# Kernel optimization log

Measured on AMD Instinct MI355X. Metric: run time of the kernel, lower is better.

Reference implementation:

```python
import jax, jax.numpy as jnp
import numpy as np

NUM_NODES = 50000
NUM_EDGES = 800000
NUM_FEATURES = 128
HIDDEN = 256
NUM_CLASSES = 10
NUM_GRAPHS = 64


def setup_inputs() -> dict:
    key = jax.random.key(0)
    ks = jax.random.split(key, 16)
    x = jax.random.normal(ks[0], (NUM_NODES, NUM_FEATURES), dtype=jnp.float32)
    edge_index = jax.random.randint(ks[1], (2, NUM_EDGES), 0, NUM_NODES, dtype=jnp.int64)
    batch = jnp.sort(jax.random.randint(ks[2], (NUM_NODES,), 0, NUM_GRAPHS, dtype=jnp.int64))

    def glorot(k, shape):
        fan_in, fan_out = shape[-2], shape[-1]
        s = jnp.sqrt(6.0 / (fan_in + fan_out)).astype(jnp.float32)
        return jax.random.uniform(k, shape, jnp.float32, -s, s)

    inp = {
        "x": x, "edge_index": edge_index, "batch": batch,
        # Chebyshev weights: one [in, out] matrix per hop order k
        "W1": glorot(ks[3], (3, NUM_FEATURES, HIDDEN)), "b1": jnp.zeros((HIDDEN,), jnp.float32),
        "W2": glorot(ks[4], (4, HIDDEN, HIDDEN)),       "b2": jnp.zeros((HIDDEN,), jnp.float32),
        "W3": glorot(ks[5], (5, HIDDEN, HIDDEN)),       "b3": jnp.zeros((HIDDEN,), jnp.float32),
        "fc1_w": glorot(ks[6], (HIDDEN, 512)),  "fc1_b": jnp.zeros((512,), jnp.float32),
        "fc2_w": glorot(ks[7], (512, HIDDEN)),  "fc2_b": jnp.zeros((HIDDEN,), jnp.float32),
        "fc3_w": glorot(ks[8], (HIDDEN, NUM_CLASSES)), "fc3_b": jnp.zeros((NUM_CLASSES,), jnp.float32),
    }
    return inp


def reference(x, edge_index, batch, W1, b1, W2, b2, W3, b3,
              fc1_w, fc1_b, fc2_w, fc2_b, fc3_w, fc3_b):
    N = x.shape[0]
    src, dst = edge_index[0], edge_index[1]

    # Scaled Laplacian L_hat = -D^{-1/2} A D^{-1/2} (lambda_max = 2, sym norm)
    deg = jax.ops.segment_sum(jnp.ones_like(src, dtype=x.dtype), src, num_segments=N)
    dis = jnp.where(deg > 0, jax.lax.rsqrt(jnp.maximum(deg, 1.0)), 0.0)
    w = -dis[src] * dis[dst]  # [E]

    def prop(h):  # L_hat @ h via gather-scale-scatter
        return jax.ops.segment_sum(h[src] * w[:, None], dst, num_segments=N)

    def cheb(h, Wk, b):
        K = Wk.shape[0]
        Tx0 = h
        out = Tx0 @ Wk[0]
        Tx1 = prop(h)
        out = out + Tx1 @ Wk[1]
        for k in range(2, K):
            Tx2 = 2.0 * prop(Tx1) - Tx0
            out = out + Tx2 @ Wk[k]
            Tx0, Tx1 = Tx1, Tx2
        return out + b

    h = jax.nn.relu(cheb(x, W1, b1))
    h = jax.nn.relu(cheb(h, W2, b2))
    h = jax.nn.relu(cheb(h, W3, b3))

    # global mean pool over graphs in the batch
    sums = jax.ops.segment_sum(h, batch, num_segments=NUM_GRAPHS)
    cnts = jax.ops.segment_sum(jnp.ones((N,), h.dtype), batch, num_segments=NUM_GRAPHS)
    g = sums / jnp.maximum(cnts, 1.0)[:, None]  # [G, 256]

    g = jax.nn.relu(g @ fc1_w + fc1_b)  # dropout is identity at inference
    g = jax.nn.relu(g @ fc2_w + fc2_b)
    g = g @ fc3_w + fc3_b
    return jax.nn.log_softmax(g, axis=1)
```

## Files before the change

kernel.cpp:

```cpp
#include <hip/hip_runtime.h>
#include <cstdint>
#include <cstddef>

#define NN 50000
#define NE 800000
#define FIN 128
#define HID 256
#define NCLS 10
#define NG 64
#define LDT 1280

#define NCH 13
#define NCELL (NN * NCH)
#define NSCB ((NCELL + 255) / 256)

typedef unsigned int uint;
typedef unsigned short ushort;
typedef __attribute__((ext_vector_type(8))) short short8;
typedef __attribute__((ext_vector_type(4))) float f32x4;

static inline size_t align_up(size_t v, size_t a) { return (v + a - 1) / a * a; }

__device__ __forceinline__ float bf2f(ushort u) {
    union { uint i; float f; } v; v.i = (uint)u << 16; return v.f;
}
__device__ __forceinline__ ushort f2bf(float f) {
    union { uint i; float f; } v; v.f = f;
    uint i = v.i;
    uint r = (i + 0x7fffu + ((i >> 16) & 1u)) >> 16;
    return (ushort)r;
}
__device__ __forceinline__ uint pack2(float a, float b) {
    return (uint)f2bf(a) | ((uint)f2bf(b) << 16);
}


__global__ void k_degcnt(const int* __restrict__ src, const int* __restrict__ dst,
                         int* __restrict__ ideg, uint* __restrict__ cellcnt32) {
    int e = blockIdx.x * 256 + threadIdx.x;
    if (e < NE) {
        int s = src[e], d = dst[e];
        atomicAdd(&ideg[s], 1);
        int cell = d * NCH + (s >> 12);
        atomicAdd(&cellcnt32[cell >> 1], 1u << ((cell & 1) * 16));
    }
}

__global__ void k_dis(const int* __restrict__ ideg, float* __restrict__ dis) {
    int n = blockIdx.x * 256 + threadIdx.x;
    if (n < NN) {
        int d = ideg[n];
        dis[n] = (d > 0) ? rsqrtf((float)d) : 0.0f;
    }
}

__global__ void k_scanA(const uint* __restrict__ cnt32, int* __restrict__ rp,
                        int* __restrict__ bsum) {
    __shared__ int s[256];
    int i = blockIdx.x * 256 + threadIdx.x;
    int v = 0;
    if (i < NCELL) v = (int)((cnt32[i >> 1] >> ((i & 1) * 16)) & 0xffffu);
    s[threadIdx.x] = v;
    __syncthreads();
    for (int off = 1; off < 256; off <<= 1) {
        int t = (threadIdx.x >= (unsigned)off) ? s[threadIdx.x - off] : 0;
        __syncthreads();
        s[threadIdx.x] += t;
        __syncthreads();
    }
    if (i < NCELL) rp[i] = s[threadIdx.x] - v;
    if (threadIdx.x == 255) bsum[blockIdx.x] = s[255];
}

__global__ void k_scanB(int* __restrict__ b, int n) {
    __shared__ int s[1024];
    __shared__ int carry;
    if (threadIdx.x == 0) carry = 0;
    __syncthreads();
    for (int base = 0; base < n; base += 1024) {
        int i = base + threadIdx.x;
        int v = (i < n) ? b[i] : 0;
        s[threadIdx.x] = v;
        __syncthreads();
        for (int off = 1; off < 1024; off <<= 1) {
            int t = (threadIdx.x >= (unsigned)off) ? s[threadIdx.x - off] : 0;
            __syncthreads();
            s[threadIdx.x] += t;
            __syncthreads();
        }
        int c = carry;
        if (i < n) b[i] = c + s[threadIdx.x] - v;
        __syncthreads();
        if (threadIdx.x == 0) carry = c + s[1023];
        __syncthreads();
    }
}

__global__ void k_scanC(const int* __restrict__ bsum, int* __restrict__ rp,
                        int* __restrict__ rpn) {
    int i = blockIdx.x * 256 + threadIdx.x;
    if (i < NCELL) {
        int v = rp[i] + bsum[blockIdx.x];
        rp[i] = v;
        if (i % NCH == 0) rpn[i / NCH] = v;
    }
    if (i == 0) rpn[NN] = NE;
}

__global__ void k_fill2(const int* __restrict__ src, const int* __restrict__ dst,
                        const float* __restrict__ dis,
                        const int* __restrict__ cellptr, uint* __restrict__ cur32,
                        uint2* __restrict__ em) {
    int e = blockIdx.x * 256 + threadIdx.x;
    if (e < NE) {
        int s = src[e], d = dst[e];
        int cell = d * NCH + (s >> 12);
        uint old = atomicAdd(&cur32[cell >> 1], 1u << ((cell & 1) * 16));
        int loc = (int)((old >> ((cell & 1) * 16)) & 0xffffu);
        uint2 m;
        m.x = (uint)s;
        m.y = __float_as_uint(-dis[s] * dis[d]);
        em[cellptr[cell] + loc] = m;
    }
}

__global__ void k_wtall(const float* __restrict__ W1, const float* __restrict__ W2,
                        const float* __restrict__ W3, ushort* __restrict__ Wt1,
                        ushort* __restrict__ Wt2, ushort* __restrict__ Wt3) {
    int i = blockIdx.x * 256 + threadIdx.x;
    if (i < 384 * 256) {
        int k = i >> 8, n = i & 255;
        Wt1[(size_t)n * 384 + k] = f2bf(W1[i]);
        return;
    }
    i -= 384 * 256;
    if (i < 1024 * 256) {
        int k = i >> 8, n = i & 255;
        Wt2[(size_t)n * 1024 + k] = f2bf(W2[i]);
        return;
    }
    i -= 1024 * 256;
    if (i < 1280 * 256) {
        int k = i >> 8, n = i & 255;
        Wt3[(size_t)n * 1280 + k] = f2bf(W3[i]);
    }
}


__global__ void k_spread_x(const float* __restrict__ x, ushort* __restrict__ T) {
    int i = blockIdx.x * 256 + threadIdx.x;
    if (i < NN * 64) {
        int m = i >> 6, p = i & 63;
        const float* xp = x + (size_t)m * FIN + p * 2;
        uint* tp = (uint*)(T + (size_t)m * LDT) + p;
        *tp = pack2(xp[0], xp[1]);
    }
}

template <int FUSE, int F>
__global__ __launch_bounds__(512) void k_prop3(
    const int* __restrict__ rpn, const uint2* __restrict__ em,
    const ushort* __restrict__ h, const ushort* __restrict__ sub,
    ushort* __restrict__ out) {
    constexpr int NV = (F == 256) ? 4 : 2;
    int wv = __builtin_amdgcn_readfirstlane(threadIdx.x >> 6);
    int d = blockIdx.x * 8 + wv;
    int lane = threadIdx.x & 63;
    int beg = rpn[d], end = rpn[d + 1];
    float a[NV];
#pragma unroll
    for (int j = 0; j < NV; ++j) a[j] = 0.0f;

    int e = beg;
    int nfull = (end - beg) >> 3;
    if (nfull > 0) {
        uint2 mt[8];
#pragma unroll
        for (int u = 0; u < 8; ++u) mt[u] = em[e + u];
        for (int g = 0; g < nfull; ++g) {
            uint2 mtn[8];
            if (F == 256) {
                uint2 gg[8];
#pragma unroll
                for (int u = 0; u < 8; ++u)
                    gg[u] = *((const uint2*)(h + (size_t)mt[u].x * LDT) + lane);
#pragma unroll
                for (int u = 0; u < 8; ++u) {
                    int pe = e + 8 + u; if (pe > end - 1) pe = end - 1;
                    mtn[u] = em[pe];
                }
#pragma unroll
                for (int u = 0; u < 8; ++u) {
                    float wvv = __uint_as_float(mt[u].y);
                    a[0] += wvv * bf2f((ushort)gg[u].x);
                    a[1] += wvv * bf2f((ushort)(gg[u].x >> 16));
                    a[2] += wvv * bf2f((ushort)gg[u].y);
                    a[3] += wvv * bf2f((ushort)(gg[u].y >> 16));
                }
            } else {
                uint gg[8];
#pragma unroll
                for (int u = 0; u < 8; ++u)
                    gg[u] = *((const uint*)(h + (size_t)mt[u].x * LDT) + lane);
#pragma unroll
                for (int u = 0; u < 8; ++u) {
                    int pe = e + 8 + u; if (pe > end - 1) pe = end - 1;
                    mtn[u] = em[pe];
                }
#pragma unroll
                for (int u = 0; u < 8; ++u) {
                    float wvv = __uint_as_float(mt[u].y);
                    a[0] += wvv * bf2f((ushort)gg[u]);
                    a[1] += wvv * bf2f((ushort)(gg[u] >> 16));
                }
            }
#pragma unroll
            for (int u = 0; u < 8; ++u) mt[u] = mtn[u];
            e += 8;
        }
    }
    for (; e + 4 <= end; e += 4) {
        uint2 mt[4];
#pragma unroll
        for (int u = 0; u < 4; ++u) mt[u] = em[e + u];
        if (F == 256) {
            uint2 gg[4];
#pragma unroll
            for (int u = 0; u < 4; ++u)
                gg[u] = *((const uint2*)(h + (size_t)mt[u].x * LDT) + lane);
#pragma unroll
            for (int u = 0; u < 4; ++u) {
                float wvv = __uint_as_float(mt[u].y);
                a[0] += wvv * bf2f((ushort)gg[u].x);
                a[1] += wvv * bf2f((ushort)(gg[u].x >> 16));
                a[2] += wvv * bf2f((ushort)gg[u].y);
                a[3] += wvv * bf2f((ushort)(gg[u].y >> 16));
            }
        } else {
            uint gg[4];
#pragma unroll
            for (int u = 0; u < 4; ++u)
                gg[u] = *((const uint*)(h + (size_t)mt[u].x * LDT) + lane);
#pragma unroll
            for (int u = 0; u < 4; ++u) {
                float wvv = __uint_as_float(mt[u].y);
                a[0] += wvv * bf2f((ushort)gg[u]);
                a[1] += wvv * bf2f((ushort)(gg[u] >> 16));
            }
        }
    }
    for (; e < end; ++e) {
        uint2 m0 = em[e];
        float w0 = __uint_as_float(m0.y);
        if (F == 256) {
            uint2 g0 = *((const uint2*)(h + (size_t)m0.x * LDT) + lane);
            a[0] += w0 * bf2f((ushort)g0.x); a[1] += w0 * bf2f((ushort)(g0.x >> 16));
            a[2] += w0 * bf2f((ushort)g0.y); a[3] += w0 * bf2f((ushort)(g0.y >> 16));
        } else {
            uint g0 = *((const uint*)(h + (size_t)m0.x * LDT) + lane);
            a[0] += w0 * bf2f((ushort)g0); a[1] += w0 * bf2f((ushort)(g0 >> 16));
        }
    }

    if (F == 256) {
        uint2* op = (uint2*)(out + (size_t)d * LDT) + lane;
        if (FUSE) {
            uint2 sv = *((const uint2*)(sub + (size_t)d * LDT) + lane);
            uint2 r;
            r.x = pack2(2.0f * a[0] - bf2f((ushort)sv.x),
                        2.0f * a[1] - bf2f((ushort)(sv.x >> 16)));
            r.y = pack2(2.0f * a[2] - bf2f((ushort)sv.y),
                        2.0f * a[3] - bf2f((ushort)(sv.y >> 16)));
            *op = r;
        } else {
            uint2 r;
            r.x = pack2(a[0], a[1]);
            r.y = pack2(a[2], a[3]);
            *op = r;
        }
    } else {
        uint* op = (uint*)(out + (size_t)d * LDT) + lane;
        if (FUSE) {
            uint sv = *((const uint*)(sub + (size_t)d * LDT) + lane);
            *op = pack2(2.0f * a[0] - bf2f((ushort)sv),
                        2.0f * a[1] - bf2f((ushort)(sv >> 16)));
        } else {
            *op = pack2(a[0], a[1]);
        }
    }
}

template <int K>
__global__ __launch_bounds__(512, 4) void k_mm7(
    const ushort* __restrict__ A, int lda,
    int m0, int m1, int m2, int m3, int m4,
    const ushort* __restrict__ Wt, const float* __restrict__ bias,
    ushort* __restrict__ H, int ldh, int M) {
    constexpr int NT = K / 32;
    __shared__ ushort As[3][128 * 32];
    __shared__ ushort Bs[3][256 * 32];
    int tid = threadIdx.x;
    int lane = tid & 63, w = tid >> 6;
    int wm = w >> 2, wn = w & 3;
    int rowBase = blockIdx.x * 128;
    int srow = lane >> 2;
    int c16 = lane & 3;

    f32x4 acc[4][4];
#pragma unroll
    for (int i = 0; i < 4; ++i)
#pragma unroll
        for (int j = 0; j < 4; ++j) acc[i][j] = (f32x4){0.f, 0.f, 0.f, 0.f};

    auto stage = [&](int t) {
        int kk = t * 32;
        int slot = kk >> 8;
        int coff = (slot == 0 ? m0 : slot == 1 ? m1 : slot == 2 ? m2
                    : slot == 3 ? m3 : m4) + (kk & 255);
        int b = t % 3;
        {
            int r = w * 16 + srow;
            int cs = c16 ^ ((r >> 1) & 3);
            int grow = rowBase + r;
            if (grow > M - 1) grow = M - 1;
            const ushort* gp = A + (size_t)grow * lda + coff + cs * 8;
            __builtin_amdgcn_global_load_lds(
                (const __attribute__((address_space(1))) void*)gp,
                (__attribute__((address_space(3))) void*)((char*)&As[b][0] + w * 1024),
                16, 0, 0);
        }
#pragma unroll
        for (int q = 0; q < 2; ++q) {
            int seg = w * 2 + q;
            int r = seg * 16 + srow;
            int cs = c16 ^ ((r >> 1) & 3);
            const ushort* gp = Wt + (size_t)r * K + kk + cs * 8;
            __builtin_amdgcn_global_load_lds(
                (const __attribute__((address_space(1))) void*)gp,
                (__attribute__((address_space(3))) void*)((char*)&Bs[b][0] + seg * 1024),
                16, 0, 0);
        }
    };

    stage(0);
    stage(1);

    for (int t = 0; t < NT; ++t) {
        if (t + 1 < NT) {
            asm volatile("s_waitcnt vmcnt(3)" ::: "memory");
        } else {
            asm volatile("s_waitcnt vmcnt(0)" ::: "memory");
        }
        __builtin_amdgcn_s_barrier();
        if (t + 2 < NT) stage(t + 2);

        int b = t % 3;
        short8 af[4], bf[4];
#pragma unroll
        for (int mi = 0; mi < 4; ++mi) {
            int r = wm * 64 + mi * 16 + (lane & 15);
            int j = (lane >> 4) ^ ((r >> 1) & 3);
            af[mi] = *(const short8*)((const char*)&As[b][0] + r * 64 + j * 16);
        }
#pragma unroll
        for (int ni = 0; ni < 4; ++ni) {
            int r = wn * 64 + ni * 16 + (lane & 15);
            int j = (lane >> 4) ^ ((r >> 1) & 3);
            bf[ni] = *(const short8*)((const char*)&Bs[b][0] + r * 64 + j * 16);
        }
#pragma unroll
        for (int mi = 0; mi < 4; ++mi)
#pragma unroll
            for (int ni = 0; ni < 4; ++ni)
                acc[mi][ni] = __builtin_amdgcn_mfma_f32_16x16x32_bf16(
                    af[mi], bf[ni], acc[mi][ni], 0, 0, 0);
    }

    int lg = lane >> 4;
    float bv[4];
#pragma unroll
    for (int ni = 0; ni < 4; ++ni)
        bv[ni] = bias[wn * 64 + ni * 16 + (lane & 15)];
#pragma unroll
    for (int mi = 0; mi < 4; ++mi) {
#pragma unroll
        for (int r = 0; r < 4; ++r) {
            int row = rowBase + wm * 64 + mi * 16 + lg * 4 + r;
            if (row >= M) continue;
#pragma unroll
            for (int ni = 0; ni < 4; ++ni) {
                int colL = wn * 64 + ni * 16 + (lane & 15);
                float v = acc[mi][ni][r] + bv[ni];
                v = fmaxf(v, 0.0f);
                H[(size_t)row * ldh + colL] = f2bf(v);
            }
        }
    }
}


__global__ void k_pool(const ushort* __restrict__ h, const int* __restrict__ batch,
                       float* __restrict__ sums, float* __restrict__ cnts) {
    int f = threadIdx.x;
    int n0 = blockIdx.x * 128;
    if (n0 >= NN) return;
    int nEnd = n0 + 128 < NN ? n0 + 128 : NN;
    int cur = batch[n0];
    float acc = 0.0f, c = 0.0f;
    for (int n = n0; n < nEnd; ++n) {
        int b = batch[n];
        if (b != cur) {
            atomicAdd(&sums[cur * HID + f], acc);
            if (f == 0) atomicAdd(&cnts[cur], c);
            acc = 0.0f; c = 0.0f; cur = b;
        }
        acc += bf2f(h[(size_t)n * HID + f]);
        c += 1.0f;
    }
    atomicAdd(&sums[cur * HID + f], acc);
    if (f == 0) atomicAdd(&cnts[cur], c);
}

__global__ void k_gdiv(const float* __restrict__ sums, const float* __restrict__ cnts,
                       float* __restrict__ g) {
    int i = blockIdx.x * 256 + threadIdx.x;
    int b = i >> 8;
    g[i] = sums[i] / fmaxf(cnts[b], 1.0f);
}


template <int RELU>
__global__ void k_fc(const float* __restrict__ in, const float* __restrict__ W,
                     const float* __restrict__ bias, float* __restrict__ out,
                     int K, int Nc) {
    __shared__ float s[512];
    int gi = blockIdx.x;
    for (int i = threadIdx.x; i < K; i += blockDim.x) s[i] = in[gi * K + i];
    __syncthreads();
    int c = blockIdx.y * blockDim.x + threadIdx.x;
    if (c < Nc) {
        float acc = bias[c];
        for (int k = 0; k < K; ++k) acc += s[k] * W[k * Nc + c];
        out[gi * Nc + c] = RELU ? fmaxf(acc, 0.0f) : acc;
    }
}

__global__ void k_fc3_lsm(const float* __restrict__ in, const float* __restrict__ W,
                          const float* __restrict__ b, float* __restrict__ out) {
    __shared__ float s[HID];
    __shared__ float lg[NCLS];
    int gi = blockIdx.x;
    s[threadIdx.x] = in[gi * HID + threadIdx.x];
    __syncthreads();
    if (threadIdx.x < NCLS) {
        float acc = b[threadIdx.x];
        for (int k = 0; k < HID; ++k) acc += s[k] * W[k * NCLS + threadIdx.x];
        lg[threadIdx.x] = acc;
    }
    __syncthreads();
    if (threadIdx.x < NCLS) {
        float m = -1e30f;
        for (int c = 0; c < NCLS; ++c) m = fmaxf(m, lg[c]);
        float sum = 0.0f;
        for (int c = 0; c < NCLS; ++c) sum += expf(lg[c] - m);
        out[gi * NCLS + threadIdx.x] = lg[threadIdx.x] - m - logf(sum);
    }
}


extern "C" void kernel_launch(void* const* d_in, const int* in_sizes, int n_in,
                              void* d_out, int out_size, void* d_ws, size_t ws_size,
                              hipStream_t stream) {
    const float* x = (const float*)d_in[0];
    const int* ei = (const int*)d_in[1];
    const int* src = ei;
    const int* dst = ei + NE;
    const int* batch = (const int*)d_in[2];
    const float* W1 = (const float*)d_in[3];
    const float* b1 = (const float*)d_in[4];
    const float* W2 = (const float*)d_in[5];
    const float* b2 = (const float*)d_in[6];
    const float* W3 = (const float*)d_in[7];
    const float* b3 = (const float*)d_in[8];
    const float* fc1w = (const float*)d_in[9];
    const float* fc1b = (const float*)d_in[10];
    const float* fc2w = (const float*)d_in[11];
    const float* fc2b = (const float*)d_in[12];
    const float* fc3w = (const float*)d_in[13];
    const float* fc3b = (const float*)d_in[14];
    float* out = (float*)d_out;

    char* p = (char*)d_ws;
    auto carve = [&](size_t bytes) {
        char* r = p;
        p += align_up(bytes, 256);
        return (void*)r;
    };
    ushort* Tbig = (ushort*)carve((size_t)NN * LDT * 2);
    ushort* hA = (ushort*)carve((size_t)NN * HID * 2);
    ushort* Wt1 = (ushort*)carve((size_t)HID * 384 * 2);
    ushort* Wt2 = (ushort*)carve((size_t)HID * 1024 * 2);
    ushort* Wt3 = (ushort*)carve((size_t)HID * 1280 * 2);
    int* ideg = (int*)carve((size_t)NN * 4);
    float* dis = (float*)carve((size_t)NN * 4);
    uint2* em = (uint2*)carve((size_t)NE * 8);
    uint* cellcnt32 = (uint*)carve((size_t)NCELL * 2);
    int* cellptr = (int*)carve((size_t)(NCELL + 1) * 4);
    uint* cur32 = (uint*)carve((size_t)NCELL * 2);
    int* rpn = (int*)carve((size_t)(NN + 1) * 4);
    int* bsum = (int*)carve((size_t)NSCB * 4);
    float* psum = (float*)carve((size_t)NG * HID * 4);
    float* pcnt = (float*)carve((size_t)NG * 4);
    float* g = (float*)carve((size_t)NG * HID * 4);
    float* f1 = (float*)carve((size_t)NG * 512 * 4);
    float* f2 = (float*)carve((size_t)NG * HID * 4);

    hipMemsetAsync(ideg, 0, (size_t)NN * 4, stream);
    hipMemsetAsync(cellcnt32, 0, (size_t)NCELL * 2, stream);
    hipMemsetAsync(cur32, 0, (size_t)NCELL * 2, stream);
    hipMemsetAsync(psum, 0, (size_t)NG * HID * 4, stream);
    hipMemsetAsync(pcnt, 0, (size_t)NG * 4, stream);

    k_degcnt<<<(NE + 255) / 256, 256, 0, stream>>>(src, dst, ideg, cellcnt32);
    k_dis<<<(NN + 255) / 256, 256, 0, stream>>>(ideg, dis);
    k_scanA<<<NSCB, 256, 0, stream>>>(cellcnt32, cellptr, bsum);
    k_scanB<<<1, 1024, 0, stream>>>(bsum, NSCB);
    k_scanC<<<NSCB, 256, 0, stream>>>(bsum, cellptr, rpn);
    k_fill2<<<(NE + 255) / 256, 256, 0, stream>>>(src, dst, dis, cellptr, cur32, em);

    k_wtall<<<(384 + 1024 + 1280), 256, 0, stream>>>(W1, W2, W3, Wt1, Wt2, Wt3);

    int mmg = (NN + 127) / 128;

    k_spread_x<<<(NN * 64 + 255) / 256, 256, 0, stream>>>(x, Tbig);
    k_prop3<0, 128><<<NN / 8, 512, 0, stream>>>(rpn, em, Tbig + 0, nullptr, Tbig + 128);
    k_prop3<1, 128><<<NN / 8, 512, 0, stream>>>(rpn, em, Tbig + 128, Tbig + 0, Tbig + 256);
    k_mm7<384><<<mmg, 512, 0, stream>>>(Tbig, LDT, 0, 256, 0, 0, 0,
                                        Wt1, b1, Tbig + 1024, LDT, NN);

    k_prop3<0, 256><<<NN / 8, 512, 0, stream>>>(rpn, em, Tbig + 1024, nullptr, Tbig + 0);
    k_prop3<1, 256><<<NN / 8, 512, 0, stream>>>(rpn, em, Tbig + 0, Tbig + 1024, Tbig + 256);
    k_prop3<1, 256><<<NN / 8, 512, 0, stream>>>(rpn, em, Tbig + 256, Tbig + 0, Tbig + 512);
    k_mm7<1024><<<mmg, 512, 0, stream>>>(Tbig, LDT, 1024, 0, 256, 512, 0,
                                         Wt2, b2, Tbig + 768, LDT, NN);

    k_prop3<0, 256><<<NN / 8, 512, 0, stream>>>(rpn, em, Tbig + 768, nullptr, Tbig + 1024);
    k_prop3<1, 256><<<NN / 8, 512, 0, stream>>>(rpn, em, Tbig + 1024, Tbig + 768, Tbig + 0);
    k_prop3<1, 256><<<NN / 8, 512, 0, stream>>>(rpn, em, Tbig + 0, Tbig + 1024, Tbig + 256);
    k_prop3<1, 256><<<NN / 8, 512, 0, stream>>>(rpn, em, Tbig + 256, Tbig + 0, Tbig + 512);
    k_mm7<1280><<<mmg, 512, 0, stream>>>(Tbig, LDT, 768, 1024, 0, 256, 512,
                                         Wt3, b3, hA, HID, NN);

    k_pool<<<(NN + 127) / 128, 256, 0, stream>>>(hA, batch, psum, pcnt);
    k_gdiv<<<(NG * HID) / 256, 256, 0, stream>>>(psum, pcnt, g);
    k_fc<1><<<dim3(NG, 2), 256, 0, stream>>>(g, fc1w, fc1b, f1, HID, 512);
    k_fc<1><<<dim3(NG, 1), 256, 0, stream>>>(f1, fc2w, fc2b, f2, 512, HID);
    k_fc3_lsm<<<NG, 256, 0, stream>>>(f2, fc3w, fc3b, out);
}
```

Baseline: 797.0 us.

## Widen 256-feature gathers to 16B half-wave loads and fuse preprocessing kernels

The 256-feature propagation kernel now splits each wavefront into two half-waves. Each half loads a full 512-byte row with 16-byte loads for alternating edges, and the partial sums are combined with a cross-half shuffle. This gives fewer, wider gather loads per edge and avoids the 4-edge tail loop. Preprocessing is also consolidated: degree counting records each edge's rank within its cell, which removes the second atomic pass and the cur32 buffer. The dis computation is merged into the scan kernel, and the edge fill, weight transpose and x conversion are merged into one launch. In exchange the kernel adds register pressure, a shuffle reduction and an odd-edge tail handled by masking.

```diff
diff --git a/kernel.cpp b/kernel.cpp
--- a/kernel.cpp
+++ b/kernel.cpp
@@ -13,6 +13,11 @@
 #define NCH 13
 #define NCELL (NN * NCH)
 #define NSCB ((NCELL + 255) / 256)
+#define NDISB ((NN + 255) / 256)
+
+#define FB 3125
+#define WTB 2688
+#define SXB 12500
 
 typedef unsigned int uint;
 typedef unsigned short ushort;
@@ -36,26 +41,29 @@
 
 
 __global__ void k_degcnt(const int* __restrict__ src, const int* __restrict__ dst,
-                         int* __restrict__ ideg, uint* __restrict__ cellcnt32) {
+                         int* __restrict__ ideg, uint* __restrict__ cellcnt32,
+                         ushort* __restrict__ rank16) {
     int e = blockIdx.x * 256 + threadIdx.x;
     if (e < NE) {
         int s = src[e], d = dst[e];
         atomicAdd(&ideg[s], 1);
         int cell = d * NCH + (s >> 12);
-        atomicAdd(&cellcnt32[cell >> 1], 1u << ((cell & 1) * 16));
-    }
-}
-
-__global__ void k_dis(const int* __restrict__ ideg, float* __restrict__ dis) {
-    int n = blockIdx.x * 256 + threadIdx.x;
-    if (n < NN) {
-        int d = ideg[n];
-        dis[n] = (d > 0) ? rsqrtf((float)d) : 0.0f;
-    }
-}
-
-__global__ void k_scanA(const uint* __restrict__ cnt32, int* __restrict__ rp,
-                        int* __restrict__ bsum) {
+        uint old = atomicAdd(&cellcnt32[cell >> 1], 1u << ((cell & 1) * 16));
+        rank16[e] = (ushort)((old >> ((cell & 1) * 16)) & 0xffffu);
+    }
+}
+
+__global__ void k_scanA_dis(const uint* __restrict__ cnt32, int* __restrict__ rp,
+                            int* __restrict__ bsum, const int* __restrict__ ideg,
+                            float* __restrict__ dis) {
+    if (blockIdx.x >= NSCB) {
+        int n = (blockIdx.x - NSCB) * 256 + threadIdx.x;
+        if (n < NN) {
+            int d = ideg[n];
+            dis[n] = (d > 0) ? rsqrtf((float)d) : 0.0f;
+        }
+        return;
+    }
     __shared__ int s[256];
     int i = blockIdx.x * 256 + threadIdx.x;
     int v = 0;
@@ -107,48 +115,49 @@
     if (i == 0) rpn[NN] = NE;
 }
 
-__global__ void k_fill2(const int* __restrict__ src, const int* __restrict__ dst,
-                        const float* __restrict__ dis,
-                        const int* __restrict__ cellptr, uint* __restrict__ cur32,
-                        uint2* __restrict__ em) {
-    int e = blockIdx.x * 256 + threadIdx.x;
-    if (e < NE) {
-        int s = src[e], d = dst[e];
-        int cell = d * NCH + (s >> 12);
-        uint old = atomicAdd(&cur32[cell >> 1], 1u << ((cell & 1) * 16));
-        int loc = (int)((old >> ((cell & 1) * 16)) & 0xffffu);
-        uint2 m;
-        m.x = (uint)s;
-        m.y = __float_as_uint(-dis[s] * dis[d]);
-        em[cellptr[cell] + loc] = m;
-    }
-}
-
-__global__ void k_wtall(const float* __restrict__ W1, const float* __restrict__ W2,
-                        const float* __restrict__ W3, ushort* __restrict__ Wt1,
-                        ushort* __restrict__ Wt2, ushort* __restrict__ Wt3) {
-    int i = blockIdx.x * 256 + threadIdx.x;
-    if (i < 384 * 256) {
-        int k = i >> 8, n = i & 255;
-        Wt1[(size_t)n * 384 + k] = f2bf(W1[i]);
+__global__ void k_fused_prep(
+    const int* __restrict__ src, const int* __restrict__ dst,
+    const float* __restrict__ dis, const int* __restrict__ cellptr,
+    const ushort* __restrict__ rank16, uint2* __restrict__ em,
+    const float* __restrict__ W1, const float* __restrict__ W2,
+    const float* __restrict__ W3, ushort* __restrict__ Wt1,
+    ushort* __restrict__ Wt2, ushort* __restrict__ Wt3,
+    const float* __restrict__ x, ushort* __restrict__ T) {
+    int b = blockIdx.x;
+    if (b < FB) {
+        int e = b * 256 + threadIdx.x;
+        if (e < NE) {
+            int s = src[e], d = dst[e];
+            int cell = d * NCH + (s >> 12);
+            int pos = cellptr[cell] + (int)rank16[e];
+            uint2 m;
+            m.x = (uint)s;
+            m.y = __float_as_uint(-dis[s] * dis[d]);
+            em[pos] = m;
+        }
         return;
     }
-    i -= 384 * 256;
-    if (i < 1024 * 256) {
-        int k = i >> 8, n = i & 255;
-        Wt2[(size_t)n * 1024 + k] = f2bf(W2[i]);
+    if (b < FB + WTB) {
+        int i = (b - FB) * 256 + threadIdx.x;
+        if (i < 384 * 256) {
+            int k = i >> 8, n = i & 255;
+            Wt1[(size_t)n * 384 + k] = f2bf(W1[i]);
+            return;
+        }
+        i -= 384 * 256;
+        if (i < 1024 * 256) {
+            int k = i >> 8, n = i & 255;
+            Wt2[(size_t)n * 1024 + k] = f2bf(W2[i]);
+            return;
+        }
+        i -= 1024 * 256;
+        if (i < 1280 * 256) {
+            int k = i >> 8, n = i & 255;
+            Wt3[(size_t)n * 1280 + k] = f2bf(W3[i]);
+        }
         return;
     }
-    i -= 1024 * 256;
-    if (i < 1280 * 256) {
-        int k = i >> 8, n = i & 255;
-        Wt3[(size_t)n * 1280 + k] = f2bf(W3[i]);
-    }
-}
-
-
-__global__ void k_spread_x(const float* __restrict__ x, ushort* __restrict__ T) {
-    int i = blockIdx.x * 256 + threadIdx.x;
+    int i = (b - FB - WTB) * 256 + threadIdx.x;
     if (i < NN * 64) {
         int m = i >> 6, p = i & 63;
         const float* xp = x + (size_t)m * FIN + p * 2;
@@ -157,19 +166,16 @@
     }
 }
 
-template <int FUSE, int F>
-__global__ __launch_bounds__(512) void k_prop3(
+template <int FUSE>
+__global__ __launch_bounds__(512) void k_prop128(
     const int* __restrict__ rpn, const uint2* __restrict__ em,
     const ushort* __restrict__ h, const ushort* __restrict__ sub,
     ushort* __restrict__ out) {
-    constexpr int NV = (F == 256) ? 4 : 2;
     int wv = __builtin_amdgcn_readfirstlane(threadIdx.x >> 6);
     int d = blockIdx.x * 8 + wv;
     int lane = threadIdx.x & 63;
     int beg = rpn[d], end = rpn[d + 1];
-    float a[NV];
-#pragma unroll
-    for (int j = 0; j < NV; ++j) a[j] = 0.0f;
+    float a0 = 0.0f, a1 = 0.0f;
 
     int e = beg;
     int nfull = (end - beg) >> 3;
@@ -179,114 +185,137 @@
         for (int u = 0; u < 8; ++u) mt[u] = em[e + u];
         for (int g = 0; g < nfull; ++g) {
             uint2 mtn[8];
-            if (F == 256) {
-                uint2 gg[8];
-#pragma unroll
-                for (int u = 0; u < 8; ++u)
-                    gg[u] = *((const uint2*)(h + (size_t)mt[u].x * LDT) + lane);
-#pragma unroll
-                for (int u = 0; u < 8; ++u) {
-                    int pe = e + 8 + u; if (pe > end - 1) pe = end - 1;
-                    mtn[u] = em[pe];
-                }
-#pragma unroll
-                for (int u = 0; u < 8; ++u) {
-                    float wvv = __uint_as_float(mt[u].y);
-                    a[0] += wvv * bf2f((ushort)gg[u].x);
-                    a[1] += wvv * bf2f((ushort)(gg[u].x >> 16));
-                    a[2] += wvv * bf2f((ushort)gg[u].y);
-                    a[3] += wvv * bf2f((ushort)(gg[u].y >> 16));
-                }
-            } else {
-                uint gg[8];
-#pragma unroll
-                for (int u = 0; u < 8; ++u)
-                    gg[u] = *((const uint*)(h + (size_t)mt[u].x * LDT) + lane);
-#pragma unroll
-                for (int u = 0; u < 8; ++u) {
-                    int pe = e + 8 + u; if (pe > end - 1) pe = end - 1;
-                    mtn[u] = em[pe];
-                }
-#pragma unroll
-                for (int u = 0; u < 8; ++u) {
-                    float wvv = __uint_as_float(mt[u].y);
-                    a[0] += wvv * bf2f((ushort)gg[u]);
-                    a[1] += wvv * bf2f((ushort)(gg[u] >> 16));
-                }
+            uint gg[8];
+#pragma unroll
+            for (int u = 0; u < 8; ++u)
+                gg[u] = *((const uint*)(h + (size_t)mt[u].x * LDT) + lane);
+#pragma unroll
+            for (int u = 0; u < 8; ++u) {
+                int pe = e + 8 + u; if (pe > end - 1) pe = end - 1;
+                mtn[u] = em[pe];
+            }
+#pragma unroll
+            for (int u = 0; u < 8; ++u) {
+                float wvv = __uint_as_float(mt[u].y);
+                a0 += wvv * bf2f((ushort)gg[u]);
+                a1 += wvv * bf2f((ushort)(gg[u] >> 16));
             }
 #pragma unroll
             for (int u = 0; u < 8; ++u) mt[u] = mtn[u];
             e += 8;
-        }
-    }
-    for (; e + 4 <= end; e += 4) {
-        uint2 mt[4];
-#pragma unroll
-        for (int u = 0; u < 4; ++u) mt[u] = em[e + u];
-        if (F == 256) {
-            uint2 gg[4];
-#pragma unroll
-            for (int u = 0; u < 4; ++u)
-                gg[u] = *((const uint2*)(h + (size_t)mt[u].x * LDT) + lane);
-#pragma unroll
-            for (int u = 0; u < 4; ++u) {
-                float wvv = __uint_as_float(mt[u].y);
-                a[0] += wvv * bf2f((ushort)gg[u].x);
-                a[1] += wvv * bf2f((ushort)(gg[u].x >> 16));
-                a[2] += wvv * bf2f((ushort)gg[u].y);
-                a[3] += wvv * bf2f((ushort)(gg[u].y >> 16));
-            }
-        } else {
-            uint gg[4];
-#pragma unroll
-            for (int u = 0; u < 4; ++u)
-                gg[u] = *((const uint*)(h + (size_t)mt[u].x * LDT) + lane);
-#pragma unroll
-            for (int u = 0; u < 4; ++u) {
-                float wvv = __uint_as_float(mt[u].y);
-                a[0] += wvv * bf2f((ushort)gg[u]);
-                a[1] += wvv * bf2f((ushort)(gg[u] >> 16));
-            }
         }
     }
     for (; e < end; ++e) {
         uint2 m0 = em[e];
         float w0 = __uint_as_float(m0.y);
-        if (F == 256) {
-            uint2 g0 = *((const uint2*)(h + (size_t)m0.x * LDT) + lane);
-            a[0] += w0 * bf2f((ushort)g0.x); a[1] += w0 * bf2f((ushort)(g0.x >> 16));
-            a[2] += w0 * bf2f((ushort)g0.y); a[3] += w0 * bf2f((ushort)(g0.y >> 16));
+        uint g0 = *((const uint*)(h + (size_t)m0.x * LDT) + lane);
+        a0 += w0 * bf2f((ushort)g0);
+        a1 += w0 * bf2f((ushort)(g0 >> 16));
+    }
+
+    uint* op = (uint*)(out + (size_t)d * LDT) + lane;
+    if (FUSE) {
+        uint sv = *((const uint*)(sub + (size_t)d * LDT) + lane);
+        *op = pack2(2.0f * a0 - bf2f((ushort)sv),
+                    2.0f * a1 - bf2f((ushort)(sv >> 16)));
+    } else {
+        *op = pack2(a0, a1);
+    }
+}
+
+template <int FUSE>
+__global__ __launch_bounds__(512) void k_prop256(
+    const int* __restrict__ rpn, const uint2* __restrict__ em,
+    const ushort* __restrict__ h, const ushort* __restrict__ sub,
+    ushort* __restrict__ out) {
+    int wv = __builtin_amdgcn_readfirstlane(threadIdx.x >> 6);
+    int d = blockIdx.x * 8 + wv;
+    int lane = threadIdx.x & 63;
+    int half = lane >> 5;
+    int l32 = lane & 31;
+    int beg = rpn[d], end = rpn[d + 1];
+    float acc[8];
+#pragma unroll
+    for (int j = 0; j < 8; ++j) acc[j] = 0.0f;
+
+    int e = beg;
+    int nb = (end - beg) >> 3;
+    if (nb > 0) {
+        uint2 mt[8];
+#pragma unroll
+        for (int u = 0; u < 8; ++u) mt[u] = em[e + u];
+        for (int g = 0; g < nb; ++g) {
+            uint2 mtn[8];
+            uint4 gv[4];
+#pragma unroll
+            for (int u = 0; u < 4; ++u) {
+                uint2 m = half ? mt[2 * u + 1] : mt[2 * u];
+                gv[u] = *((const uint4*)(h + (size_t)m.x * LDT) + l32);
+            }
+#pragma unroll
+            for (int u = 0; u < 8; ++u) {
+                int pe = e + 8 + u; if (pe > end - 1) pe = end - 1;
+                mtn[u] = em[pe];
+            }
+#pragma unroll
+            for (int u = 0; u < 4; ++u) {
+                uint2 m = half ? mt[2 * u + 1] : mt[2 * u];
+                float w = __uint_as_float(m.y);
+                acc[0] += w * bf2f((ushort)gv[u].x);
+                acc[1] += w * bf2f((ushort)(gv[u].x >> 16));
+                acc[2] += w * bf2f((ushort)gv[u].y);
+                acc[3] += w * bf2f((ushort)(gv[u].y >> 16));
+                acc[4] += w * bf2f((ushort)gv[u].z);
+                acc[5] += w * bf2f((ushort)(gv[u].z >> 16));
+                acc[6] += w * bf2f((ushort)gv[u].w);
+                acc[7] += w * bf2f((ushort)(gv[u].w >> 16));
+            }
+#pragma unroll
+            for (int u = 0; u < 8; ++u) mt[u] = mtn[u];
+            e += 8;
+        }
+    }
+    for (; e + 2 <= end; e += 2) {
+        uint2 m = half ? em[e + 1] : em[e];
+        uint4 gvv = *((const uint4*)(h + (size_t)m.x * LDT) + l32);
+        float w = __uint_as_float(m.y);
+        acc[0] += w * bf2f((ushort)gvv.x); acc[1] += w * bf2f((ushort)(gvv.x >> 16));
+        acc[2] += w * bf2f((ushort)gvv.y); acc[3] += w * bf2f((ushort)(gvv.y >> 16));
+        acc[4] += w * bf2f((ushort)gvv.z); acc[5] += w * bf2f((ushort)(gvv.z >> 16));
+        acc[6] += w * bf2f((ushort)gvv.w); acc[7] += w * bf2f((ushort)(gvv.w >> 16));
+    }
+    if (e < end) {
+        uint2 m = em[e];
+        uint4 gvv = *((const uint4*)(h + (size_t)m.x * LDT) + l32);
+        float w = half ? 0.0f : __uint_as_float(m.y);
+        acc[0] += w * bf2f((ushort)gvv.x); acc[1] += w * bf2f((ushort)(gvv.x >> 16));
+        acc[2] += w * bf2f((ushort)gvv.y); acc[3] += w * bf2f((ushort)(gvv.y >> 16));
+        acc[4] += w * bf2f((ushort)gvv.z); acc[5] += w * bf2f((ushort)(gvv.z >> 16));
+        acc[6] += w * bf2f((ushort)gvv.w); acc[7] += w * bf2f((ushort)(gvv.w >> 16));
+    }
+#pragma unroll
+    for (int j = 0; j < 8; ++j) acc[j] += __shfl_xor(acc[j], 32);
+
+    if (half == 0) {
+        uint4* op = (uint4*)(out + (size_t)d * LDT) + l32;
+        uint4 r;
+        if (FUSE) {
+            uint4 sv = *((const uint4*)(sub + (size_t)d * LDT) + l32);
+            r.x = pack2(2.0f * acc[0] - bf2f((ushort)sv.x),
+                        2.0f * acc[1] - bf2f((ushort)(sv.x >> 16)));
+            r.y = pack2(2.0f * acc[2] - bf2f((ushort)sv.y),
+                        2.0f * acc[3] - bf2f((ushort)(sv.y >> 16)));
+            r.z = pack2(2.0f * acc[4] - bf2f((ushort)sv.z),
+                        2.0f * acc[5] - bf2f((ushort)(sv.z >> 16)));
+            r.w = pack2(2.0f * acc[6] - bf2f((ushort)sv.w),
+                        2.0f * acc[7] - bf2f((ushort)(sv.w >> 16)));
         } else {
-            uint g0 = *((const uint*)(h + (size_t)m0.x * LDT) + lane);
-            a[0] += w0 * bf2f((ushort)g0); a[1] += w0 * bf2f((ushort)(g0 >> 16));
-        }
-    }
-
-    if (F == 256) {
-        uint2* op = (uint2*)(out + (size_t)d * LDT) + lane;
-        if (FUSE) {
-            uint2 sv = *((const uint2*)(sub + (size_t)d * LDT) + lane);
-            uint2 r;
-            r.x = pack2(2.0f * a[0] - bf2f((ushort)sv.x),
-                        2.0f * a[1] - bf2f((ushort)(sv.x >> 16)));
-            r.y = pack2(2.0f * a[2] - bf2f((ushort)sv.y),
-                        2.0f * a[3] - bf2f((ushort)(sv.y >> 16)));
-            *op = r;
-        } else {
-            uint2 r;
-            r.x = pack2(a[0], a[1]);
-            r.y = pack2(a[2], a[3]);
-            *op = r;
-        }
-    } else {
-        uint* op = (uint*)(out + (size_t)d * LDT) + lane;
-        if (FUSE) {
-            uint sv = *((const uint*)(sub + (size_t)d * LDT) + lane);
-            *op = pack2(2.0f * a[0] - bf2f((ushort)sv),
-                        2.0f * a[1] - bf2f((ushort)(sv >> 16)));
-        } else {
-            *op = pack2(a[0], a[1]);
-        }
+            r.x = pack2(acc[0], acc[1]);
+            r.y = pack2(acc[2], acc[3]);
+            r.z = pack2(acc[4], acc[5]);
+            r.w = pack2(acc[6], acc[7]);
+        }
+        *op = r;
     }
 }
 
@@ -506,7 +535,7 @@
     uint2* em = (uint2*)carve((size_t)NE * 8);
     uint* cellcnt32 = (uint*)carve((size_t)NCELL * 2);
     int* cellptr = (int*)carve((size_t)(NCELL + 1) * 4);
-    uint* cur32 = (uint*)carve((size_t)NCELL * 2);
+    ushort* rank16 = (ushort*)carve((size_t)NE * 2);
     int* rpn = (int*)carve((size_t)(NN + 1) * 4);
     int* bsum = (int*)carve((size_t)NSCB * 4);
     float* psum = (float*)carve((size_t)NG * HID * 4);
@@ -517,37 +546,34 @@
 
     hipMemsetAsync(ideg, 0, (size_t)NN * 4, stream);
     hipMemsetAsync(cellcnt32, 0, (size_t)NCELL * 2, stream);
-    hipMemsetAsync(cur32, 0, (size_t)NCELL * 2, stream);
     hipMemsetAsync(psum, 0, (size_t)NG * HID * 4, stream);
     hipMemsetAsync(pcnt, 0, (size_t)NG * 4, stream);
 
-    k_degcnt<<<(NE + 255) / 256, 256, 0, stream>>>(src, dst, ideg, cellcnt32);
-    k_dis<<<(NN + 255) / 256, 256, 0, stream>>>(ideg, dis);
-    k_scanA<<<NSCB, 256, 0, stream>>>(cellcnt32, cellptr, bsum);
+    k_degcnt<<<(NE + 255) / 256, 256, 0, stream>>>(src, dst, ideg, cellcnt32, rank16);
+    k_scanA_dis<<<NSCB + NDISB, 256, 0, stream>>>(cellcnt32, cellptr, bsum, ideg, dis);
     k_scanB<<<1, 1024, 0, stream>>>(bsum, NSCB);
     k_scanC<<<NSCB, 256, 0, stream>>>(bsum, cellptr, rpn);
-    k_fill2<<<(NE + 255) / 256, 256, 0, stream>>>(src, dst, dis, cellptr, cur32, em);
-
-    k_wtall<<<(384 + 1024 + 1280), 256, 0, stream>>>(W1, W2, W3, Wt1, Wt2, Wt3);
+    k_fused_prep<<<FB + WTB + SXB, 256, 0, stream>>>(
+        src, dst, dis, cellptr, rank16, em,
+        W1, W2, W3, Wt1, Wt2, Wt3, x, Tbig);
 
     int mmg = (NN + 127) / 128;
 
-    k_spread_x<<<(NN * 64 + 255) / 256, 256, 0, stream>>>(x, Tbig);
-    k_prop3<0, 128><<<NN / 8, 512, 0, stream>>>(rpn, em, Tbig + 0, nullptr, Tbig + 128);
-    k_prop3<1, 128><<<NN / 8, 512, 0, stream>>>(rpn, em, Tbig + 128, Tbig + 0, Tbig + 256);
+    k_prop128<0><<<NN / 8, 512, 0, stream>>>(rpn, em, Tbig + 0, nullptr, Tbig + 128);
+    k_prop128<1><<<NN / 8, 512, 0, stream>>>(rpn, em, Tbig + 128, Tbig + 0, Tbig + 256);
     k_mm7<384><<<mmg, 512, 0, stream>>>(Tbig, LDT, 0, 256, 0, 0, 0,
                                         Wt1, b1, Tbig + 1024, LDT, NN);
 
-    k_prop3<0, 256><<<NN / 8, 512, 0, stream>>>(rpn, em, Tbig + 1024, nullptr, Tbig + 0);
-    k_prop3<1, 256><<<NN / 8, 512, 0, stream>>>(rpn, em, Tbig + 0, Tbig + 1024, Tbig + 256);
-    k_prop3<1, 256><<<NN / 8, 512, 0, stream>>>(rpn, em, Tbig + 256, Tbig + 0, Tbig + 512);
+    k_prop256<0><<<NN / 8, 512, 0, stream>>>(rpn, em, Tbig + 1024, nullptr, Tbig + 0);
+    k_prop256<1><<<NN / 8, 512, 0, stream>>>(rpn, em, Tbig + 0, Tbig + 1024, Tbig + 256);
+    k_prop256<1><<<NN / 8, 512, 0, stream>>>(rpn, em, Tbig + 256, Tbig + 0, Tbig + 512);
     k_mm7<1024><<<mmg, 512, 0, stream>>>(Tbig, LDT, 1024, 0, 256, 512, 0,
                                          Wt2, b2, Tbig + 768, LDT, NN);
 
-    k_prop3<0, 256><<<NN / 8, 512, 0, stream>>>(rpn, em, Tbig + 768, nullptr, Tbig + 1024);
-    k_prop3<1, 256><<<NN / 8, 512, 0, stream>>>(rpn, em, Tbig + 1024, Tbig + 768, Tbig + 0);
-    k_prop3<1, 256><<<NN / 8, 512, 0, stream>>>(rpn, em, Tbig + 0, Tbig + 1024, Tbig + 256);
-    k_prop3<1, 256><<<NN / 8, 512, 0, stream>>>(rpn, em, Tbig + 256, Tbig + 0, Tbig + 512);
+    k_prop256<0><<<NN / 8, 512, 0, stream>>>(rpn, em, Tbig + 768, nullptr, Tbig + 1024);
+    k_prop256<1><<<NN / 8, 512, 0, stream>>>(rpn, em, Tbig + 1024, Tbig + 768, Tbig + 0);
+    k_prop256<1><<<NN / 8, 512, 0, stream>>>(rpn, em, Tbig + 0, Tbig + 1024, Tbig + 256);
+    k_prop256<1><<<NN / 8, 512, 0, stream>>>(rpn, em, Tbig + 256, Tbig + 0, Tbig + 512);
     k_mm7<1280><<<mmg, 512, 0, stream>>>(Tbig, LDT, 768, 1024, 0, 256, 512,
                                          Wt3, b3, hA, HID, NN);
 
```

New measurement: 931.7 us. +16.9%, slower.

## Record edge ranks during counting and fuse preprocessing kernels into fewer launches

Applied to the files above, without the earlier changes.

The per-cell rank returned by the counting atomic is now stored in a 16-bit array, so the fill pass no longer needs a second atomic pass over a separate cursor array or its memset. The degree-normalisation kernel is merged into the first scan kernel as extra blocks. The edge fill, weight transpose and input spreading are combined into a single block-partitioned kernel. The aim is fewer launches and atomics in the preprocessing stage, at the cost of an extra per-edge 16-bit buffer write and read.

```diff
diff --git a/kernel.cpp b/kernel.cpp
--- a/kernel.cpp
+++ b/kernel.cpp
@@ -13,6 +13,11 @@
 #define NCH 13
 #define NCELL (NN * NCH)
 #define NSCB ((NCELL + 255) / 256)
+#define NDISB ((NN + 255) / 256)
+
+#define FB 3125
+#define WTB 2688
+#define SXB 12500
 
 typedef unsigned int uint;
 typedef unsigned short ushort;
@@ -36,26 +41,29 @@
 
 
 __global__ void k_degcnt(const int* __restrict__ src, const int* __restrict__ dst,
-                         int* __restrict__ ideg, uint* __restrict__ cellcnt32) {
+                         int* __restrict__ ideg, uint* __restrict__ cellcnt32,
+                         ushort* __restrict__ rank16) {
     int e = blockIdx.x * 256 + threadIdx.x;
     if (e < NE) {
         int s = src[e], d = dst[e];
         atomicAdd(&ideg[s], 1);
         int cell = d * NCH + (s >> 12);
-        atomicAdd(&cellcnt32[cell >> 1], 1u << ((cell & 1) * 16));
-    }
-}
-
-__global__ void k_dis(const int* __restrict__ ideg, float* __restrict__ dis) {
-    int n = blockIdx.x * 256 + threadIdx.x;
-    if (n < NN) {
-        int d = ideg[n];
-        dis[n] = (d > 0) ? rsqrtf((float)d) : 0.0f;
-    }
-}
-
-__global__ void k_scanA(const uint* __restrict__ cnt32, int* __restrict__ rp,
-                        int* __restrict__ bsum) {
+        uint old = atomicAdd(&cellcnt32[cell >> 1], 1u << ((cell & 1) * 16));
+        rank16[e] = (ushort)((old >> ((cell & 1) * 16)) & 0xffffu);
+    }
+}
+
+__global__ void k_scanA_dis(const uint* __restrict__ cnt32, int* __restrict__ rp,
+                            int* __restrict__ bsum, const int* __restrict__ ideg,
+                            float* __restrict__ dis) {
+    if (blockIdx.x >= NSCB) {
+        int n = (blockIdx.x - NSCB) * 256 + threadIdx.x;
+        if (n < NN) {
+            int d = ideg[n];
+            dis[n] = (d > 0) ? rsqrtf((float)d) : 0.0f;
+        }
+        return;
+    }
     __shared__ int s[256];
     int i = blockIdx.x * 256 + threadIdx.x;
     int v = 0;
@@ -107,48 +115,49 @@
     if (i == 0) rpn[NN] = NE;
 }
 
-__global__ void k_fill2(const int* __restrict__ src, const int* __restrict__ dst,
-                        const float* __restrict__ dis,
-                        const int* __restrict__ cellptr, uint* __restrict__ cur32,
-                        uint2* __restrict__ em) {
-    int e = blockIdx.x * 256 + threadIdx.x;
-    if (e < NE) {
-        int s = src[e], d = dst[e];
-        int cell = d * NCH + (s >> 12);
-        uint old = atomicAdd(&cur32[cell >> 1], 1u << ((cell & 1) * 16));
-        int loc = (int)((old >> ((cell & 1) * 16)) & 0xffffu);
-        uint2 m;
-        m.x = (uint)s;
-        m.y = __float_as_uint(-dis[s] * dis[d]);
-        em[cellptr[cell] + loc] = m;
-    }
-}
-
-__global__ void k_wtall(const float* __restrict__ W1, const float* __restrict__ W2,
-                        const float* __restrict__ W3, ushort* __restrict__ Wt1,
-                        ushort* __restrict__ Wt2, ushort* __restrict__ Wt3) {
-    int i = blockIdx.x * 256 + threadIdx.x;
-    if (i < 384 * 256) {
-        int k = i >> 8, n = i & 255;
-        Wt1[(size_t)n * 384 + k] = f2bf(W1[i]);
+__global__ void k_fused_prep(
+    const int* __restrict__ src, const int* __restrict__ dst,
+    const float* __restrict__ dis, const int* __restrict__ cellptr,
+    const ushort* __restrict__ rank16, uint2* __restrict__ em,
+    const float* __restrict__ W1, const float* __restrict__ W2,
+    const float* __restrict__ W3, ushort* __restrict__ Wt1,
+    ushort* __restrict__ Wt2, ushort* __restrict__ Wt3,
+    const float* __restrict__ x, ushort* __restrict__ T) {
+    int b = blockIdx.x;
+    if (b < FB) {
+        int e = b * 256 + threadIdx.x;
+        if (e < NE) {
+            int s = src[e], d = dst[e];
+            int cell = d * NCH + (s >> 12);
+            int pos = cellptr[cell] + (int)rank16[e];
+            uint2 m;
+            m.x = (uint)s;
+            m.y = __float_as_uint(-dis[s] * dis[d]);
+            em[pos] = m;
+        }
         return;
     }
-    i -= 384 * 256;
-    if (i < 1024 * 256) {
-        int k = i >> 8, n = i & 255;
-        Wt2[(size_t)n * 1024 + k] = f2bf(W2[i]);
+    if (b < FB + WTB) {
+        int i = (b - FB) * 256 + threadIdx.x;
+        if (i < 384 * 256) {
+            int k = i >> 8, n = i & 255;
+            Wt1[(size_t)n * 384 + k] = f2bf(W1[i]);
+            return;
+        }
+        i -= 384 * 256;
+        if (i < 1024 * 256) {
+            int k = i >> 8, n = i & 255;
+            Wt2[(size_t)n * 1024 + k] = f2bf(W2[i]);
+            return;
+        }
+        i -= 1024 * 256;
+        if (i < 1280 * 256) {
+            int k = i >> 8, n = i & 255;
+            Wt3[(size_t)n * 1280 + k] = f2bf(W3[i]);
+        }
         return;
     }
-    i -= 1024 * 256;
-    if (i < 1280 * 256) {
-        int k = i >> 8, n = i & 255;
-        Wt3[(size_t)n * 1280 + k] = f2bf(W3[i]);
-    }
-}
-
-
-__global__ void k_spread_x(const float* __restrict__ x, ushort* __restrict__ T) {
-    int i = blockIdx.x * 256 + threadIdx.x;
+    int i = (b - FB - WTB) * 256 + threadIdx.x;
     if (i < NN * 64) {
         int m = i >> 6, p = i & 63;
         const float* xp = x + (size_t)m * FIN + p * 2;
@@ -506,7 +515,7 @@
     uint2* em = (uint2*)carve((size_t)NE * 8);
     uint* cellcnt32 = (uint*)carve((size_t)NCELL * 2);
     int* cellptr = (int*)carve((size_t)(NCELL + 1) * 4);
-    uint* cur32 = (uint*)carve((size_t)NCELL * 2);
+    ushort* rank16 = (ushort*)carve((size_t)NE * 2);
     int* rpn = (int*)carve((size_t)(NN + 1) * 4);
     int* bsum = (int*)carve((size_t)NSCB * 4);
     float* psum = (float*)carve((size_t)NG * HID * 4);
@@ -517,22 +526,19 @@
 
     hipMemsetAsync(ideg, 0, (size_t)NN * 4, stream);
     hipMemsetAsync(cellcnt32, 0, (size_t)NCELL * 2, stream);
-    hipMemsetAsync(cur32, 0, (size_t)NCELL * 2, stream);
     hipMemsetAsync(psum, 0, (size_t)NG * HID * 4, stream);
     hipMemsetAsync(pcnt, 0, (size_t)NG * 4, stream);
 
-    k_degcnt<<<(NE + 255) / 256, 256, 0, stream>>>(src, dst, ideg, cellcnt32);
-    k_dis<<<(NN + 255) / 256, 256, 0, stream>>>(ideg, dis);
-    k_scanA<<<NSCB, 256, 0, stream>>>(cellcnt32, cellptr, bsum);
+    k_degcnt<<<(NE + 255) / 256, 256, 0, stream>>>(src, dst, ideg, cellcnt32, rank16);
+    k_scanA_dis<<<NSCB + NDISB, 256, 0, stream>>>(cellcnt32, cellptr, bsum, ideg, dis);
     k_scanB<<<1, 1024, 0, stream>>>(bsum, NSCB);
     k_scanC<<<NSCB, 256, 0, stream>>>(bsum, cellptr, rpn);
-    k_fill2<<<(NE + 255) / 256, 256, 0, stream>>>(src, dst, dis, cellptr, cur32, em);
-
-    k_wtall<<<(384 + 1024 + 1280), 256, 0, stream>>>(W1, W2, W3, Wt1, Wt2, Wt3);
+    k_fused_prep<<<FB + WTB + SXB, 256, 0, stream>>>(
+        src, dst, dis, cellptr, rank16, em,
+        W1, W2, W3, Wt1, Wt2, Wt3, x, Tbig);
 
     int mmg = (NN + 127) / 128;
 
-    k_spread_x<<<(NN * 64 + 255) / 256, 256, 0, stream>>>(x, Tbig);
     k_prop3<0, 128><<<NN / 8, 512, 0, stream>>>(rpn, em, Tbig + 0, nullptr, Tbig + 128);
     k_prop3<1, 128><<<NN / 8, 512, 0, stream>>>(rpn, em, Tbig + 128, Tbig + 0, Tbig + 256);
     k_mm7<384><<<mmg, 512, 0, stream>>>(Tbig, LDT, 0, 256, 0, 0, 0,
```

Measured after the change: 781.7 us. Within noise of the previous version (-1.9%).
